# Kernel tuning notes

Hardware: AMD Instinct MI355X
Metric: run time of the kernel (lower is better)

The kernel has to match this reference:

```python
import jax, jax.numpy as jnp
import numpy as np

MARGIN = 0.2
BIG = 1e9  # sentinel for masked (positive-pair) entries in the row-min


def setup_inputs() -> dict:
    key = jax.random.key(0)
    k1, k2, k3 = jax.random.split(key, 3)
    B, D, NUM_CLASSES = 4096, 512, 1000
    z_s = jax.random.normal(k1, (B, D), dtype=jnp.float32)
    z_i = jax.random.normal(k2, (B, D), dtype=jnp.float32)
    labels = jax.random.randint(k3, (B,), 0, NUM_CLASSES, dtype=jnp.int64)
    return {"z_s": z_s, "z_i": z_i, "labels": labels}


def reference(z_s, z_i, labels):
    # dists[a, b] = 1 - <z_s[a], z_i[b]>   -- [B, B]
    dists = 1.0 - jnp.einsum("ad,bd->ab", z_s, z_i)
    pos_mask = labels[:, None] == labels[None, :]  # [B, B] same-label pairs

    p = jnp.diagonal(dists)  # positive distance per anchor, [B]
    # hardest negative per anchor: min over entries with different label
    n = jnp.min(jnp.where(pos_mask, BIG, dists), axis=1)  # [B]
    has_neg = ~jnp.all(pos_mask, axis=1)  # anchors with at least one negative

    per_anchor = jax.nn.relu(p - n + MARGIN)  # [B]
    count = jnp.sum(has_neg)
    total = jnp.sum(jnp.where(has_neg, per_anchor, 0.0))
    # mean over anchors that had negatives; 0.0 if none (matches torch fallback)
    return jnp.where(count > 0, total / jnp.maximum(count, 1).astype(total.dtype), 0.0)
```

## Files before the change

kernel.cpp:

```cpp
#include <hip/hip_runtime.h>
#include <hip/hip_bf16.h>

typedef __attribute__((ext_vector_type(8))) short bf16x8;
typedef __attribute__((ext_vector_type(4))) float f32x4;

#define NB 4096
#define ND 512
#define MARGIN_F 0.2f

__device__ __forceinline__ unsigned int enc_f32(float f) {
    unsigned int b = __float_as_uint(f);
    return (b & 0x80000000u) ? ~b : (b | 0x80000000u);
}

__device__ __forceinline__ float dec_f32(unsigned int e) {
    unsigned int b = (e & 0x80000000u) ? (e & 0x7fffffffu) : ~e;
    return __uint_as_float(b);
}

__device__ __forceinline__ void gld_lds16(const void* g, void* l) {
    __builtin_amdgcn_global_load_lds((__attribute__((address_space(1))) void*)g,
                                     (__attribute__((address_space(3))) void*)l,
                                     16, 0, 0);
}

__device__ __forceinline__ float selv(f32x4 v, int r) {
    float s01 = (r & 1) ? v[1] : v[0];
    float s23 = (r & 1) ? v[3] : v[2];
    return (r & 2) ? s23 : s01;
}

__global__ __launch_bounds__(256) void k_prep(const float* __restrict__ zs,
                                              const float* __restrict__ zi,
                                              __hip_bfloat16* __restrict__ outb,
                                              unsigned int* __restrict__ rowmax) {
    const int bid = blockIdx.x;
    if (bid < 16) rowmax[bid * 256 + threadIdx.x] = 0u;

    int gid = bid * 256 + threadIdx.x;
    int mat = gid >> 18;
    int t   = gid & 0x3FFFF;
    int si  = t >> 6;
    int L   = t & 63;
    const float* src = mat ? zi : zs;
    int row = ((si >> 4) << 4) | (L & 15);
    int col = ((si & 15) << 5) | (((L >> 4) & 3) << 3);
    const float4* p = (const float4*)(src + (size_t)row * ND + col);
    float4 f0 = p[0];
    float4 f1 = p[1];
    union { __hip_bfloat16 h[8]; bf16x8 v; } u;
    u.h[0] = __float2bfloat16(f0.x);
    u.h[1] = __float2bfloat16(f0.y);
    u.h[2] = __float2bfloat16(f0.z);
    u.h[3] = __float2bfloat16(f0.w);
    u.h[4] = __float2bfloat16(f1.x);
    u.h[5] = __float2bfloat16(f1.y);
    u.h[6] = __float2bfloat16(f1.z);
    u.h[7] = __float2bfloat16(f1.w);
    bf16x8* dst = (bf16x8*)(outb + ((size_t)mat << 21) + ((size_t)si << 9) + (L << 3));
    *dst = u.v;
}

__global__ __launch_bounds__(512, 2) void k_gemm_rowmax(const __hip_bfloat16* __restrict__ zsb,
                                                        const __hip_bfloat16* __restrict__ zib,
                                                        const int* __restrict__ labels,
                                                        unsigned int* __restrict__ rowmax,
                                                        float* __restrict__ p_diag) {
    __shared__ __align__(16) unsigned char lds[131072];
    __shared__ int labA[256];
    __shared__ int labB[256];

    const int tid = threadIdx.x;
    const int bid = blockIdx.x;
    const int xcd = bid & 7, lid = bid >> 3;
    const int bx = ((xcd & 3) << 2) | (lid & 3);
    const int by = ((xcd >> 2) << 3) | (lid >> 2);

    if (tid < 256) labA[tid] = labels[by * 256 + tid];
    else           labB[tid & 255] = labels[bx * 256 + (tid - 256)];

    const char* gA = (const char*)zsb;
    const char* gB = (const char*)zib;
    const int rbw = tid >> 6;
    const int cw  = (tid & 63) << 4;
    const int aQ = by * 16;
    const int bQ = bx * 16;

#define STAGEQ(kt, q) do {                                                         \
        size_t _gc = ((size_t)((((kt) << 1) | (q)) << 10)) + cw;                   \
        unsigned _ld = (((kt) & 1) << 16) + ((q) << 14) + (tid << 4);              \
        gld_lds16(gA + (((size_t)(aQ + rbw))     << 14) + _gc, lds + _ld);         \
        gld_lds16(gA + (((size_t)(aQ + 8 + rbw)) << 14) + _gc, lds + _ld + 8192);  \
        gld_lds16(gB + (((size_t)(bQ + rbw))     << 14) + _gc, lds + _ld + 32768); \
        gld_lds16(gB + (((size_t)(bQ + 8 + rbw)) << 14) + _gc, lds + _ld + 40960); \
    } while (0)

    const int w = tid >> 6, lane = tid & 63;
    const int w_m = w >> 2, w_n = w & 3;
    const unsigned fragOff = (unsigned)(lane << 4);
    const unsigned aBase2 = (unsigned)(w_m << 13) + fragOff;
    const unsigned bBase2 = 32768u + (unsigned)(w_n << 12) + fragOff;

    const f32x4 Z4 = (f32x4){0.f, 0.f, 0.f, 0.f};
    f32x4 acc00=Z4, acc01=Z4, acc02=Z4, acc03=Z4;
    f32x4 acc10=Z4, acc11=Z4, acc12=Z4, acc13=Z4;
    f32x4 acc20=Z4, acc21=Z4, acc22=Z4, acc23=Z4;
    f32x4 acc30=Z4, acc31=Z4, acc32=Z4, acc33=Z4;
    f32x4 acc40=Z4, acc41=Z4, acc42=Z4, acc43=Z4;
    f32x4 acc50=Z4, acc51=Z4, acc52=Z4, acc53=Z4;
    f32x4 acc60=Z4, acc61=Z4, acc62=Z4, acc63=Z4;
    f32x4 acc70=Z4, acc71=Z4, acc72=Z4, acc73=Z4;
    bf16x8 a_0, a_1, a_2, a_3, b_0, b_1, b_2, b_3;

#define MF(A, B, C) __builtin_amdgcn_mfma_f32_16x16x32_bf16((A), (B), (C), 0, 0, 0)
#define LDBq(q)                                                                     \
    b_0 = *(const bf16x8*)(lds + par + ((q) << 14) + bBase2 + (0 << 10));           \
    b_1 = *(const bf16x8*)(lds + par + ((q) << 14) + bBase2 + (1 << 10));           \
    b_2 = *(const bf16x8*)(lds + par + ((q) << 14) + bBase2 + (2 << 10));           \
    b_3 = *(const bf16x8*)(lds + par + ((q) << 14) + bBase2 + (3 << 10));
#define LDAq(mh, q)                                                                 \
    a_0 = *(const bf16x8*)(lds + par + ((q) << 14) + aBase2 + ((((mh) << 2) + 0) << 10)); \
    a_1 = *(const bf16x8*)(lds + par + ((q) << 14) + aBase2 + ((((mh) << 2) + 1) << 10)); \
    a_2 = *(const bf16x8*)(lds + par + ((q) << 14) + aBase2 + ((((mh) << 2) + 2) << 10)); \
    a_3 = *(const bf16x8*)(lds + par + ((q) << 14) + aBase2 + ((((mh) << 2) + 3) << 10));
#define ROW4(A, R)                                                             \
    acc##R##0 = MF((A), b_0, acc##R##0);                                       \
    acc##R##1 = MF((A), b_1, acc##R##1);                                       \
    acc##R##2 = MF((A), b_2, acc##R##2);                                       \
    acc##R##3 = MF((A), b_3, acc##R##3);
#define PHASE_SYNC()                                                           \
    __builtin_amdgcn_s_barrier();                                              \
    asm volatile("s_waitcnt lgkmcnt(0)" ::: "memory");                         \
    __builtin_amdgcn_sched_barrier(0);

    STAGEQ(0, 0); STAGEQ(0, 1);
    __syncthreads();

#pragma unroll
    for (int kt = 0; kt < 8; ++kt) {
        const unsigned par = (unsigned)((kt & 1) << 16);

        LDBq(0)
        LDAq(0, 0)
        if (kt < 7) STAGEQ(kt + 1, 0);
        PHASE_SYNC()
        __builtin_amdgcn_s_setprio(1);
        ROW4(a_0, 0) ROW4(a_1, 1) ROW4(a_2, 2) ROW4(a_3, 3)
        __builtin_amdgcn_s_setprio(0);
        __builtin_amdgcn_s_barrier();

        LDAq(1, 0)
        PHASE_SYNC()
        __builtin_amdgcn_s_setprio(1);
        ROW4(a_0, 4) ROW4(a_1, 5) ROW4(a_2, 6) ROW4(a_3, 7)
        __builtin_amdgcn_s_setprio(0);
        if (kt < 7) asm volatile("s_waitcnt vmcnt(4)" ::: "memory");
        else        asm volatile("s_waitcnt vmcnt(0)" ::: "memory");
        __builtin_amdgcn_s_barrier();

        LDBq(1)
        LDAq(0, 1)
        if (kt < 7) STAGEQ(kt + 1, 1);
        PHASE_SYNC()
        __builtin_amdgcn_s_setprio(1);
        ROW4(a_0, 0) ROW4(a_1, 1) ROW4(a_2, 2) ROW4(a_3, 3)
        __builtin_amdgcn_s_setprio(0);
        __builtin_amdgcn_s_barrier();

        LDAq(1, 1)
        PHASE_SYNC()
        __builtin_amdgcn_s_setprio(1);
        ROW4(a_0, 4) ROW4(a_1, 5) ROW4(a_2, 6) ROW4(a_3, 7)
        __builtin_amdgcn_s_setprio(0);
        if (kt < 7) asm volatile("s_waitcnt vmcnt(4)" ::: "memory");
        __builtin_amdgcn_s_barrier();
    }
#undef STAGEQ
#undef LDAq
#undef LDBq
#undef ROW4
#undef PHASE_SYNC

    const int quad = lane >> 4;
    const int lcol = lane & 15;
    const int epiBase = by * 256 + w_m * 128 + quad * 4;

    const int lb_0 = labB[w_n * 64 + 0 * 16 + lcol];
    const int lb_1 = labB[w_n * 64 + 1 * 16 + lcol];
    const int lb_2 = labB[w_n * 64 + 2 * 16 + lcol];
    const int lb_3 = labB[w_n * 64 + 3 * 16 + lcol];

#define EPIV(m, n, LB) {                                                       \
        float v0 = acc##m##n[0], v1 = acc##m##n[1];                            \
        float v2 = acc##m##n[2], v3 = acc##m##n[3];                            \
        if (la0 != (LB) && v0 > mx0) mx0 = v0;                                 \
        if (la1 != (LB) && v1 > mx1) mx1 = v1;                                 \
        if (la2 != (LB) && v2 > mx2) mx2 = v2;                                 \
        if (la3 != (LB) && v3 > mx3) mx3 = v3; }
#define EPIRED(m, r, MX) {                                                     \
        float mm = (MX);                                                       \
        mm = fmaxf(mm, __shfl_xor(mm, 1));                                     \
        mm = fmaxf(mm, __shfl_xor(mm, 2));                                     \
        mm = fmaxf(mm, __shfl_xor(mm, 4));                                     \
        mm = fmaxf(mm, __shfl_xor(mm, 8));                                     \
        if (lcol == 0 && mm > -2.9e38f)                                        \
            atomicMax(&rowmax[epiBase + (m) * 16 + (r)], enc_f32(mm)); }
#define EPIMS(m) {                                                             \
        int la0 = labA[w_m * 128 + (m) * 16 + quad * 4 + 0];                   \
        int la1 = labA[w_m * 128 + (m) * 16 + quad * 4 + 1];                   \
        int la2 = labA[w_m * 128 + (m) * 16 + quad * 4 + 2];                   \
        int la3 = labA[w_m * 128 + (m) * 16 + quad * 4 + 3];                   \
        float mx0 = -3.0e38f, mx1 = -3.0e38f, mx2 = -3.0e38f, mx3 = -3.0e38f;  \
        EPIV(m, 0, lb_0) EPIV(m, 1, lb_1) EPIV(m, 2, lb_2) EPIV(m, 3, lb_3)    \
        EPIRED(m, 0, mx0) EPIRED(m, 1, mx1) EPIRED(m, 2, mx2) EPIRED(m, 3, mx3) }

    EPIMS(0) EPIMS(1) EPIMS(2) EPIMS(3)
    EPIMS(4) EPIMS(5) EPIMS(6) EPIMS(7)
#undef EPIMS
#undef EPIRED
#undef EPIV

    if (bx == by && (w_n >> 1) == w_m && (lcol >> 2) == quad) {
        int r = lcol & 3;
        f32x4 d0 = (w_n & 1) ? acc40 : acc00;
        f32x4 d1 = (w_n & 1) ? acc51 : acc11;
        f32x4 d2 = (w_n & 1) ? acc62 : acc22;
        f32x4 d3 = (w_n & 1) ? acc73 : acc33;
        int base = by * 256 + w_m * 128 + ((w_n & 1) << 6) + lcol;
        p_diag[base +  0] = 1.0f - selv(d0, r);
        p_diag[base + 16] = 1.0f - selv(d1, r);
        p_diag[base + 32] = 1.0f - selv(d2, r);
        p_diag[base + 48] = 1.0f - selv(d3, r);
    }
}

__global__ __launch_bounds__(1024) void k_finalize(const unsigned int* __restrict__ rowmax,
                                                   const float* __restrict__ p_diag,
                                                   float* __restrict__ out) {
    int tid = threadIdx.x;
    float sum = 0.0f;
    int cnt = 0;
#pragma unroll
    for (int it = 0; it < 4; ++it) {
        int a = tid + it * 1024;
        unsigned int e = rowmax[a];
        if (e != 0u) {
            float n = 1.0f - dec_f32(e);
            float per = p_diag[a] - n + MARGIN_F;
            if (per > 0.0f) sum += per;
            cnt++;
        }
    }
#pragma unroll
    for (int off = 32; off > 0; off >>= 1) {
        sum += __shfl_xor(sum, off);
        cnt += __shfl_xor(cnt, off);
    }
    __shared__ float sSum[16];
    __shared__ int sCnt[16];
    int w = tid >> 6, lane = tid & 63;
    if (lane == 0) { sSum[w] = sum; sCnt[w] = cnt; }
    __syncthreads();
    if (tid == 0) {
        float ts = 0.0f;
        int tc = 0;
#pragma unroll
        for (int i = 0; i < 16; ++i) { ts += sSum[i]; tc += sCnt[i]; }
        out[0] = (tc > 0) ? ts / (float)tc : 0.0f;
    }
}

extern "C" void kernel_launch(void* const* d_in, const int* in_sizes, int n_in,
                              void* d_out, int out_size, void* d_ws, size_t ws_size,
                              hipStream_t stream) {
    (void)in_sizes; (void)n_in; (void)out_size; (void)ws_size;
    const float* zs = (const float*)d_in[0];
    const float* zi = (const float*)d_in[1];
    const int* labels = (const int*)d_in[2];
    float* out = (float*)d_out;

    char* ws = (char*)d_ws;
    __hip_bfloat16* zb = (__hip_bfloat16*)ws;
    unsigned int* rowmax = (unsigned int*)(ws + (8u << 20));
    float* p_diag = (float*)(ws + (8u << 20) + 16384);

    k_prep<<<2048, 256, 0, stream>>>(zs, zi, zb, rowmax);
    dim3 g(256);
    k_gemm_rowmax<<<g, 512, 0, stream>>>(zb, zb + (size_t)NB * ND, labels, rowmax, p_diag);
    k_finalize<<<1, 1024, 0, stream>>>(rowmax, p_diag, out);
}
```

Before: 99.48 us.

## Shrink GEMM tile to 128x128 with 4 waves and simpler double-buffered pipeline

Replaces the 256x256-tile, 8-wave GEMM that used a hand-scheduled quarter-phase pipeline with a 128x128 tile computed by 4 waves, launched as 1024 blocks instead of 256. The K loop becomes plain double buffering: prefetch the next stage, then compute, with one __syncthreads per iteration. The explicit barriers, waitcnts and setprio calls are removed. The aim is more blocks per CU and better load balance across 256 CUs, at the cost of lower data reuse per tile, more global and L2 traffic, and less tuned latency hiding.

Result: slower. 102.2 us (+2.7%).

```diff
diff --git a/kernel.cpp b/kernel.cpp
--- a/kernel.cpp
+++ b/kernel.cpp
@@ -61,129 +61,99 @@
     *dst = u.v;
 }
 
-__global__ __launch_bounds__(512, 2) void k_gemm_rowmax(const __hip_bfloat16* __restrict__ zsb,
+__global__ __launch_bounds__(256, 2) void k_gemm_rowmax(const __hip_bfloat16* __restrict__ zsb,
                                                         const __hip_bfloat16* __restrict__ zib,
                                                         const int* __restrict__ labels,
                                                         unsigned int* __restrict__ rowmax,
                                                         float* __restrict__ p_diag) {
-    __shared__ __align__(16) unsigned char lds[131072];
-    __shared__ int labA[256];
-    __shared__ int labB[256];
+    __shared__ __align__(16) unsigned char lds[65536];
+    __shared__ int labA[128];
+    __shared__ int labB[128];
 
     const int tid = threadIdx.x;
     const int bid = blockIdx.x;
     const int xcd = bid & 7, lid = bid >> 3;
-    const int bx = ((xcd & 3) << 2) | (lid & 3);
-    const int by = ((xcd >> 2) << 3) | (lid >> 2);
-
-    if (tid < 256) labA[tid] = labels[by * 256 + tid];
-    else           labB[tid & 255] = labels[bx * 256 + (tid - 256)];
+    const int bx = ((xcd & 1) << 4) | (lid & 15);
+    const int by = ((xcd >> 1) << 3) | (lid >> 4);
+
+    if (tid < 128) labA[tid] = labels[by * 128 + tid];
+    else           labB[tid - 128] = labels[bx * 128 + (tid - 128)];
 
     const char* gA = (const char*)zsb;
     const char* gB = (const char*)zib;
     const int rbw = tid >> 6;
     const int cw  = (tid & 63) << 4;
-    const int aQ = by * 16;
-    const int bQ = bx * 16;
-
-#define STAGEQ(kt, q) do {                                                         \
-        size_t _gc = ((size_t)((((kt) << 1) | (q)) << 10)) + cw;                   \
-        unsigned _ld = (((kt) & 1) << 16) + ((q) << 14) + (tid << 4);              \
-        gld_lds16(gA + (((size_t)(aQ + rbw))     << 14) + _gc, lds + _ld);         \
-        gld_lds16(gA + (((size_t)(aQ + 8 + rbw)) << 14) + _gc, lds + _ld + 8192);  \
-        gld_lds16(gB + (((size_t)(bQ + rbw))     << 14) + _gc, lds + _ld + 32768); \
-        gld_lds16(gB + (((size_t)(bQ + 8 + rbw)) << 14) + _gc, lds + _ld + 40960); \
+    const int q_t = rbw & 1;
+    const int rb_t = rbw >> 1;
+    const int aQ = by * 8;
+    const int bQ = bx * 8;
+
+#define STAGE(kt) do {                                                             \
+        size_t _gc = ((size_t)(((kt) << 1) + q_t) << 10) + cw;                     \
+        unsigned _ld = (((kt) & 1) << 14) + (tid << 4);                            \
+        gld_lds16(gA + (((size_t)(aQ + 0 + rb_t)) << 14) + _gc, lds + _ld);        \
+        gld_lds16(gA + (((size_t)(aQ + 2 + rb_t)) << 14) + _gc, lds + _ld + 4096); \
+        gld_lds16(gA + (((size_t)(aQ + 4 + rb_t)) << 14) + _gc, lds + _ld + 8192); \
+        gld_lds16(gA + (((size_t)(aQ + 6 + rb_t)) << 14) + _gc, lds + _ld + 12288);\
+        gld_lds16(gB + (((size_t)(bQ + 0 + rb_t)) << 14) + _gc, lds + 32768 + _ld);\
+        gld_lds16(gB + (((size_t)(bQ + 2 + rb_t)) << 14) + _gc, lds + 32768 + _ld + 4096); \
+        gld_lds16(gB + (((size_t)(bQ + 4 + rb_t)) << 14) + _gc, lds + 32768 + _ld + 8192); \
+        gld_lds16(gB + (((size_t)(bQ + 6 + rb_t)) << 14) + _gc, lds + 32768 + _ld + 12288);\
     } while (0)
 
     const int w = tid >> 6, lane = tid & 63;
-    const int w_m = w >> 2, w_n = w & 3;
+    const int w_m = w >> 1, w_n = w & 1;
     const unsigned fragOff = (unsigned)(lane << 4);
-    const unsigned aBase2 = (unsigned)(w_m << 13) + fragOff;
-    const unsigned bBase2 = 32768u + (unsigned)(w_n << 12) + fragOff;
+    const unsigned aBase = (unsigned)(w_m << 13) + fragOff;
+    const unsigned bBase = 32768u + (unsigned)(w_n << 13) + fragOff;
 
     const f32x4 Z4 = (f32x4){0.f, 0.f, 0.f, 0.f};
     f32x4 acc00=Z4, acc01=Z4, acc02=Z4, acc03=Z4;
     f32x4 acc10=Z4, acc11=Z4, acc12=Z4, acc13=Z4;
     f32x4 acc20=Z4, acc21=Z4, acc22=Z4, acc23=Z4;
     f32x4 acc30=Z4, acc31=Z4, acc32=Z4, acc33=Z4;
-    f32x4 acc40=Z4, acc41=Z4, acc42=Z4, acc43=Z4;
-    f32x4 acc50=Z4, acc51=Z4, acc52=Z4, acc53=Z4;
-    f32x4 acc60=Z4, acc61=Z4, acc62=Z4, acc63=Z4;
-    f32x4 acc70=Z4, acc71=Z4, acc72=Z4, acc73=Z4;
     bf16x8 a_0, a_1, a_2, a_3, b_0, b_1, b_2, b_3;
 
 #define MF(A, B, C) __builtin_amdgcn_mfma_f32_16x16x32_bf16((A), (B), (C), 0, 0, 0)
-#define LDBq(q)                                                                     \
-    b_0 = *(const bf16x8*)(lds + par + ((q) << 14) + bBase2 + (0 << 10));           \
-    b_1 = *(const bf16x8*)(lds + par + ((q) << 14) + bBase2 + (1 << 10));           \
-    b_2 = *(const bf16x8*)(lds + par + ((q) << 14) + bBase2 + (2 << 10));           \
-    b_3 = *(const bf16x8*)(lds + par + ((q) << 14) + bBase2 + (3 << 10));
-#define LDAq(mh, q)                                                                 \
-    a_0 = *(const bf16x8*)(lds + par + ((q) << 14) + aBase2 + ((((mh) << 2) + 0) << 10)); \
-    a_1 = *(const bf16x8*)(lds + par + ((q) << 14) + aBase2 + ((((mh) << 2) + 1) << 10)); \
-    a_2 = *(const bf16x8*)(lds + par + ((q) << 14) + aBase2 + ((((mh) << 2) + 2) << 10)); \
-    a_3 = *(const bf16x8*)(lds + par + ((q) << 14) + aBase2 + ((((mh) << 2) + 3) << 10));
+#define LDBq(q)                                                                \
+    b_0 = *(const bf16x8*)(lds + par + bBase + 0 * 2048 + ((q) << 10));        \
+    b_1 = *(const bf16x8*)(lds + par + bBase + 1 * 2048 + ((q) << 10));        \
+    b_2 = *(const bf16x8*)(lds + par + bBase + 2 * 2048 + ((q) << 10));        \
+    b_3 = *(const bf16x8*)(lds + par + bBase + 3 * 2048 + ((q) << 10));
+#define LDAq(q)                                                                \
+    a_0 = *(const bf16x8*)(lds + par + aBase + 0 * 2048 + ((q) << 10));        \
+    a_1 = *(const bf16x8*)(lds + par + aBase + 1 * 2048 + ((q) << 10));        \
+    a_2 = *(const bf16x8*)(lds + par + aBase + 2 * 2048 + ((q) << 10));        \
+    a_3 = *(const bf16x8*)(lds + par + aBase + 3 * 2048 + ((q) << 10));
 #define ROW4(A, R)                                                             \
     acc##R##0 = MF((A), b_0, acc##R##0);                                       \
     acc##R##1 = MF((A), b_1, acc##R##1);                                       \
     acc##R##2 = MF((A), b_2, acc##R##2);                                       \
     acc##R##3 = MF((A), b_3, acc##R##3);
-#define PHASE_SYNC()                                                           \
-    __builtin_amdgcn_s_barrier();                                              \
-    asm volatile("s_waitcnt lgkmcnt(0)" ::: "memory");                         \
-    __builtin_amdgcn_sched_barrier(0);
-
-    STAGEQ(0, 0); STAGEQ(0, 1);
+
+    STAGE(0);
     __syncthreads();
 
 #pragma unroll
     for (int kt = 0; kt < 8; ++kt) {
-        const unsigned par = (unsigned)((kt & 1) << 16);
-
+        const unsigned par = (unsigned)((kt & 1) << 14);
+        if (kt < 7) STAGE(kt + 1);
         LDBq(0)
-        LDAq(0, 0)
-        if (kt < 7) STAGEQ(kt + 1, 0);
-        PHASE_SYNC()
-        __builtin_amdgcn_s_setprio(1);
+        LDAq(0)
         ROW4(a_0, 0) ROW4(a_1, 1) ROW4(a_2, 2) ROW4(a_3, 3)
-        __builtin_amdgcn_s_setprio(0);
-        __builtin_amdgcn_s_barrier();
-
-        LDAq(1, 0)
-        PHASE_SYNC()
-        __builtin_amdgcn_s_setprio(1);
-        ROW4(a_0, 4) ROW4(a_1, 5) ROW4(a_2, 6) ROW4(a_3, 7)
-        __builtin_amdgcn_s_setprio(0);
-        if (kt < 7) asm volatile("s_waitcnt vmcnt(4)" ::: "memory");
-        else        asm volatile("s_waitcnt vmcnt(0)" ::: "memory");
-        __builtin_amdgcn_s_barrier();
-
         LDBq(1)
-        LDAq(0, 1)
-        if (kt < 7) STAGEQ(kt + 1, 1);
-        PHASE_SYNC()
-        __builtin_amdgcn_s_setprio(1);
+        LDAq(1)
         ROW4(a_0, 0) ROW4(a_1, 1) ROW4(a_2, 2) ROW4(a_3, 3)
-        __builtin_amdgcn_s_setprio(0);
-        __builtin_amdgcn_s_barrier();
-
-        LDAq(1, 1)
-        PHASE_SYNC()
-        __builtin_amdgcn_s_setprio(1);
-        ROW4(a_0, 4) ROW4(a_1, 5) ROW4(a_2, 6) ROW4(a_3, 7)
-        __builtin_amdgcn_s_setprio(0);
-        if (kt < 7) asm volatile("s_waitcnt vmcnt(4)" ::: "memory");
-        __builtin_amdgcn_s_barrier();
-    }
-#undef STAGEQ
+        if (kt < 7) __syncthreads();
+    }
+#undef STAGE
 #undef LDAq
 #undef LDBq
 #undef ROW4
-#undef PHASE_SYNC
 
     const int quad = lane >> 4;
     const int lcol = lane & 15;
-    const int epiBase = by * 256 + w_m * 128 + quad * 4;
+    const int epiBase = by * 128 + w_m * 64 + quad * 4;
 
     const int lb_0 = labB[w_n * 64 + 0 * 16 + lcol];
     const int lb_1 = labB[w_n * 64 + 1 * 16 + lcol];
@@ -206,31 +176,26 @@
         if (lcol == 0 && mm > -2.9e38f)                                        \
             atomicMax(&rowmax[epiBase + (m) * 16 + (r)], enc_f32(mm)); }
 #define EPIMS(m) {                                                             \
-        int la0 = labA[w_m * 128 + (m) * 16 + quad * 4 + 0];                   \
-        int la1 = labA[w_m * 128 + (m) * 16 + quad * 4 + 1];                   \
-        int la2 = labA[w_m * 128 + (m) * 16 + quad * 4 + 2];                   \
-        int la3 = labA[w_m * 128 + (m) * 16 + quad * 4 + 3];                   \
+        int la0 = labA[w_m * 64 + (m) * 16 + quad * 4 + 0];                    \
+        int la1 = labA[w_m * 64 + (m) * 16 + quad * 4 + 1];                    \
+        int la2 = labA[w_m * 64 + (m) * 16 + quad * 4 + 2];                    \
+        int la3 = labA[w_m * 64 + (m) * 16 + quad * 4 + 3];                    \
         float mx0 = -3.0e38f, mx1 = -3.0e38f, mx2 = -3.0e38f, mx3 = -3.0e38f;  \
         EPIV(m, 0, lb_0) EPIV(m, 1, lb_1) EPIV(m, 2, lb_2) EPIV(m, 3, lb_3)    \
         EPIRED(m, 0, mx0) EPIRED(m, 1, mx1) EPIRED(m, 2, mx2) EPIRED(m, 3, mx3) }
 
     EPIMS(0) EPIMS(1) EPIMS(2) EPIMS(3)
-    EPIMS(4) EPIMS(5) EPIMS(6) EPIMS(7)
 #undef EPIMS
 #undef EPIRED
 #undef EPIV
 
-    if (bx == by && (w_n >> 1) == w_m && (lcol >> 2) == quad) {
+    if (bx == by && w_m == w_n && (lcol >> 2) == quad) {
         int r = lcol & 3;
-        f32x4 d0 = (w_n & 1) ? acc40 : acc00;
-        f32x4 d1 = (w_n & 1) ? acc51 : acc11;
-        f32x4 d2 = (w_n & 1) ? acc62 : acc22;
-        f32x4 d3 = (w_n & 1) ? acc73 : acc33;
-        int base = by * 256 + w_m * 128 + ((w_n & 1) << 6) + lcol;
-        p_diag[base +  0] = 1.0f - selv(d0, r);
-        p_diag[base + 16] = 1.0f - selv(d1, r);
-        p_diag[base + 32] = 1.0f - selv(d2, r);
-        p_diag[base + 48] = 1.0f - selv(d3, r);
+        int base = by * 128 + w_m * 64 + lcol;
+        p_diag[base +  0] = 1.0f - selv(acc00, r);
+        p_diag[base + 16] = 1.0f - selv(acc11, r);
+        p_diag[base + 32] = 1.0f - selv(acc22, r);
+        p_diag[base + 48] = 1.0f - selv(acc33, r);
     }
 }
 
@@ -285,7 +250,6 @@
     float* p_diag = (float*)(ws + (8u << 20) + 16384);
 
     k_prep<<<2048, 256, 0, stream>>>(zs, zi, zb, rowmax);
-    dim3 g(256);
-    k_gemm_rowmax<<<g, 512, 0, stream>>>(zb, zb + (size_t)NB * ND, labels, rowmax, p_diag);
+    k_gemm_rowmax<<<1024, 256, 0, stream>>>(zb, zb + (size_t)NB * ND, labels, rowmax, p_diag);
     k_finalize<<<1, 1024, 0, stream>>>(rowmax, p_diag, out);
 }
```
